# Optimization experiments

Measured on AMD Instinct MI355X. Metric: run time of the kernel, lower is better.

The kernel has to match this reference:

```python
import jax, jax.numpy as jnp
import numpy as np

EPS = 1e-5

def layer_norm(x, g, b):
    mu = jnp.mean(x, axis=-1, keepdims=True)
    var = jnp.mean(jnp.square(x - mu), axis=-1, keepdims=True)
    return (x - mu) * jax.lax.rsqrt(var + EPS) * g + b

def setup_inputs() -> dict:
    key = jax.random.key(0)
    B, N, IN_D, S, D = 64, 4096, 256, 8, 256
    ks = jax.random.split(key, 20)
    scale = lambda fan_in: 1.0 / np.sqrt(fan_in)
    u = lambda k, shape, s: jax.random.uniform(k, shape, jnp.float32, -s, s)
    return {
        "inputs": jax.random.normal(ks[0], (B, N, IN_D), jnp.float32),
        "noise": jax.random.normal(ks[1], (B, S, D), jnp.float32),
        "slots_mu": jax.random.normal(ks[2], (1, S, D), jnp.float32),
        "slots_sigma": jnp.ones((1, S, D), jnp.float32) * 0.1,
        "Wq": u(ks[3], (D, D), scale(D)), "bq": u(ks[4], (D,), scale(D)),
        "Wk": u(ks[5], (D, IN_D), scale(IN_D)), "bk": u(ks[6], (D,), scale(IN_D)),
        "Wv": u(ks[7], (D, IN_D), scale(IN_D)), "bv": u(ks[8], (D,), scale(IN_D)),
        "W_ih": u(ks[9], (3 * D, D), scale(D)), "b_ih": u(ks[10], (3 * D,), scale(D)),
        "W_hh": u(ks[11], (3 * D, D), scale(D)), "b_hh": u(ks[12], (3 * D,), scale(D)),
        "W1": u(ks[13], (D, D), scale(D)), "b1": u(ks[14], (D,), scale(D)),
        "W2": u(ks[15], (D, D), scale(D)), "b2": u(ks[16], (D,), scale(D)),
        "ln_slots_g": jnp.ones((D,), jnp.float32), "ln_slots_b": jnp.zeros((D,), jnp.float32),
        "ln_mlp_g": jnp.ones((D,), jnp.float32), "ln_mlp_b": jnp.zeros((D,), jnp.float32),
    }

def gru_cell(x, h, W_ih, b_ih, W_hh, b_hh):
    # PyTorch GRUCell: gates ordered (reset, update, new)
    gi = x @ W_ih.T + b_ih  # [B*S, 3D]
    gh = h @ W_hh.T + b_hh
    i_r, i_z, i_n = jnp.split(gi, 3, axis=-1)
    h_r, h_z, h_n = jnp.split(gh, 3, axis=-1)
    r = jax.nn.sigmoid(i_r + h_r)
    z = jax.nn.sigmoid(i_z + h_z)
    n = jnp.tanh(i_n + r * h_n)
    return (1.0 - z) * n + z * h

def reference(inputs, noise, slots_mu, slots_sigma, Wq, bq, Wk, bk, Wv, bv,
              W_ih, b_ih, W_hh, b_hh, W1, b1, W2, b2,
              ln_slots_g, ln_slots_b, ln_mlp_g, ln_mlp_b):
    B, N, _ = inputs.shape
    _, S, D = noise.shape
    num_iterations = 3
    slots = slots_mu + slots_sigma * noise  # [B, S, D]
    # k, v are loop-invariant; hoist the big GEMMs out of the iteration loop
    k = jnp.einsum('bnd,ed->bne', inputs, Wk) + bk  # [B, N, D]
    v = jnp.einsum('bnd,ed->bne', inputs, Wv) + bv  # [B, N, D]
    inv_sqrt_d = 1.0 / np.sqrt(D)
    for _ in range(num_iterations):
        slots_prev = slots
        q = layer_norm(slots, ln_slots_g, ln_slots_b) @ Wq.T + bq  # [B, S, D]
        attn_logits = jnp.einsum('bsd,bnd->bsn', q, k) * inv_sqrt_d
        attn = jax.nn.softmax(attn_logits, axis=-1)  # softmax over inputs (dim=-1)
        updates = jnp.einsum('bsn,bnd->bsd', attn, v)  # [B, S, D]
        h_new = gru_cell(updates.reshape(-1, D), slots_prev.reshape(-1, D),
                         W_ih, b_ih, W_hh, b_hh).reshape(B, S, D)
        slots = slots_prev + h_new  # residual around GRU (as in source)
        hidden = jax.nn.relu(layer_norm(slots, ln_mlp_g, ln_mlp_b) @ W1.T + b1)
        slots = slots + (hidden @ W2.T + b2)
    return slots
```

## Files before the change

kernel.cpp:

```cpp
#include <hip/hip_runtime.h>


constexpr int Bn = 64;
constexpr int Nn = 4096;
constexpr int Dd = 256;
constexpr int Ss = 8;
constexpr int CH = 16;
constexpr float EPSF = 1e-5f;

#define DEV __device__ __forceinline__

using short8 = __attribute__((ext_vector_type(8))) short;
using f32x4 = __attribute__((ext_vector_type(4))) float;
union U8 { short8 s; uint4 u; };

DEV unsigned bfpack2(float lo, float hi) {
  unsigned ul = __float_as_uint(lo), uh = __float_as_uint(hi);
  ul = (ul + 0x7FFFu + ((ul >> 16) & 1u)) >> 16;
  uh = (uh + 0x7FFFu + ((uh >> 16) & 1u)) & 0xFFFF0000u;
  return ul | uh;
}
DEV unsigned short bf16r(float x) {
  unsigned u = __float_as_uint(x);
  u = (u + 0x7FFFu + ((u >> 16) & 1u)) >> 16;
  return (unsigned short)u;
}
DEV float rsum32(float v) {
  v += __shfl_xor(v, 1); v += __shfl_xor(v, 2); v += __shfl_xor(v, 4);
  v += __shfl_xor(v, 8); v += __shfl_xor(v, 16);
  return v;
}
DEV float sigm(float x) { return 1.f / (1.f + __expf(-x)); }

template <int NK>
DEV void load_af(short8* a, const unsigned short* base, int lda, int m16, int quad) {
  const unsigned short* p = base + m16 * lda + quad * 8;
#pragma unroll
  for (int kk = 0; kk < NK; ++kk) a[kk] = *(const short8*)(p + kk * 32);
}
template <int NK>
DEV f32x4 gemm_tile(const short8* a, const unsigned short* wr, float binit) {
  f32x4 acc = {binit, binit, binit, binit};
#pragma unroll
  for (int kk = 0; kk < NK; ++kk) {
    short8 b = *(const short8*)(wr + kk * 32);
    acc = __builtin_amdgcn_mfma_f32_16x16x32_bf16(a[kk], b, acc, 0, 0, 0);
  }
  return acc;
}

DEV void ln_row8(const float* x, const float* g, const float* b, int d0,
                 unsigned short* dst) {
  float s = x[0] + x[1] + x[2] + x[3] + x[4] + x[5] + x[6] + x[7];
  float mu = rsum32(s) * (1.f / 256.f);
  float q = 0.f;
#pragma unroll
  for (int j = 0; j < 8; ++j) { float d = x[j] - mu; q += d * d; }
  float rs = rsqrtf(rsum32(q) * (1.f / 256.f) + EPSF);
  float o[8];
#pragma unroll
  for (int j = 0; j < 8; ++j) o[j] = (x[j] - mu) * rs * g[d0 + j] + b[d0 + j];
  uint4 w;
  w.x = bfpack2(o[0], o[1]); w.y = bfpack2(o[2], o[3]);
  w.z = bfpack2(o[4], o[5]); w.w = bfpack2(o[6], o[7]);
  *(uint4*)dst = w;
}

__global__ __launch_bounds__(256) void k_init(const float* __restrict__ noise,
                                              const float* __restrict__ mu,
                                              const float* __restrict__ sg,
                                              float* __restrict__ slots) {
  int i = blockIdx.x * 256 + threadIdx.x;
  float4 nz = ((const float4*)noise)[i];
  int m = i & 511;
  float4 m4 = ((const float4*)mu)[m];
  float4 s4 = ((const float4*)sg)[m];
  float4 o;
  o.x = m4.x + s4.x * nz.x; o.y = m4.y + s4.y * nz.y;
  o.z = m4.z + s4.z * nz.z; o.w = m4.w + s4.w * nz.w;
  ((float4*)slots)[i] = o;
}

__global__ __launch_bounds__(256) void k_wqk(const float* __restrict__ Wq,
                                             const float* __restrict__ Wk,
                                             const float* __restrict__ bq,
                                             float* __restrict__ WqkT,
                                             float* __restrict__ bqk) {
  int tid = threadIdx.x, c = blockIdx.x;
  if (c < 256) {
    float acc = 0.f;
    for (int e = 0; e < 256; ++e) acc += Wq[e * 256 + tid] * Wk[e * 256 + c];
    WqkT[c * 256 + tid] = acc;
  } else {
    float acc = 0.f;
    for (int e = 0; e < 256; ++e) acc += bq[e] * Wk[e * 256 + tid];
    bqk[tid] = acc;
  }
}

__global__ __launch_bounds__(256) void k_conv(
    const float* __restrict__ Wv, const float* __restrict__ Wih,
    const float* __restrict__ Whh, const float* __restrict__ W1,
    const float* __restrict__ W2, const float* __restrict__ WqkT,
    const float* __restrict__ bih, const float* __restrict__ bhh,
    unsigned* Wv_b, unsigned* Wzr_b, unsigned* Win_b, unsigned* Whn_b,
    unsigned* W1_b, unsigned* W2_b, unsigned* Wqk_b, float* bzr) {
  if (blockIdx.x >= 1280) {
    int i = (blockIdx.x - 1280) * 256 + threadIdx.x;
    if (i < 512) bzr[i] = bih[i] + bhh[i];
    return;
  }
  int p = blockIdx.x * 256 + threadIdx.x;
  const float* src; unsigned* dst;
  if (p < 32768) { src = Wv + 2 * p; dst = Wv_b + p; }
  else if (p < 163840) {
    int q = p - 32768, row = q >> 8, col = (q & 255) * 2;
    src = (col < 256) ? (Wih + row * 256 + col) : (Whh + row * 256 + col - 256);
    dst = Wzr_b + q;
  }
  else if (p < 196608) { int q = p - 163840; src = Wih + 512 * 256 + 2 * q; dst = Win_b + q; }
  else if (p < 229376) { int q = p - 196608; src = Whh + 512 * 256 + 2 * q; dst = Whn_b + q; }
  else if (p < 262144) { int q = p - 229376; src = W1 + 2 * q; dst = W1_b + q; }
  else if (p < 294912) { int q = p - 262144; src = W2 + 2 * q; dst = W2_b + q; }
  else { int q = p - 294912; src = WqkT + 2 * q; dst = Wqk_b + q; }
  dst[0] = bfpack2(src[0], src[1]);
}

__global__ __launch_bounds__(512) void k_qk0(const float* __restrict__ slots,
                                             const float* __restrict__ gsl,
                                             const float* __restrict__ bsl,
                                             const unsigned short* __restrict__ Wqk_b,
                                             const float* __restrict__ bqk,
                                             float* __restrict__ qk) {
  __shared__ __align__(16) unsigned short lnb[16 * 264];
  const int tid = threadIdx.x, bb = blockIdx.x;
  const int lane = tid & 63, wave = tid >> 6;
  const int m16 = lane & 15, quad = lane >> 4;
  const int row = tid >> 5, l32 = tid & 31, d0 = l32 * 8;
  {
    const float* sp = slots + (size_t)(bb * 16 + row) * 256 + d0;
    float4 v0 = *(const float4*)sp, v1 = *(const float4*)(sp + 4);
    float x[8] = {v0.x, v0.y, v0.z, v0.w, v1.x, v1.y, v1.z, v1.w};
    ln_row8(x, gsl, bsl, d0, lnb + row * 264 + d0);
  }
  __syncthreads();
  short8 a8[8];
  load_af<8>(a8, lnb, 264, m16, quad);
#pragma unroll
  for (int i = 0; i < 2; ++i) {
    int t = wave + 8 * i;
    f32x4 acc = gemm_tile<8>(a8, Wqk_b + (size_t)(t * 16 + m16) * 256 + quad * 8,
                             bqk[t * 16 + m16]);
#pragma unroll
    for (int r = 0; r < 4; ++r)
      qk[(size_t)(bb * 16 + quad * 4 + r) * 256 + t * 16 + m16] = acc[r] * 0.0625f;
  }
}

template <bool FIRST>
DEV void ld_chunk(const float* __restrict__ xin, unsigned* __restrict__ xbf,
                  size_t nbase, int tid, uint4* pr) {
#pragma unroll
  for (int i = 0; i < 4; ++i) {
    int flat = i * 256 + tid, n = flat >> 5, od = flat & 31;
    if (FIRST) {
      const float4* src = (const float4*)(xin + (nbase + n) * 256 + od * 8);
      float4 v0 = src[0], v1 = src[1];
      uint4 o;
      o.x = bfpack2(v0.x, v0.y); o.y = bfpack2(v0.z, v0.w);
      o.z = bfpack2(v1.x, v1.y); o.w = bfpack2(v1.z, v1.w);
      ((uint4*)xbf)[(nbase + n) * 32 + od] = o;
      pr[i] = o;
    } else {
      pr[i] = ((const uint4*)xbf)[(nbase + n) * 32 + od];
    }
  }
}

template <bool FIRST>
__global__ __launch_bounds__(256) void k_attn(const float* __restrict__ xin,
                                              unsigned* __restrict__ xbf,
                                              const float* __restrict__ qk,
                                              float* __restrict__ pl,
                                              float* __restrict__ pu) {
  __shared__ __align__(16) unsigned xt[2][128 * 33];
  __shared__ __align__(16) unsigned pp[16 * 17];
  __shared__ __align__(16) float lred[2][16];
  const int tid = threadIdx.x;
  const int lane = tid & 63, wave = tid >> 6;
  const int m16 = lane & 15, quad = lane >> 4;
  const int c = blockIdx.x, b = blockIdx.y;
  const int pb = (b * CH + c) * 8;

  short8 aq[8];
  {
    const float* qrow = qk + (size_t)(b * 8 + (m16 & 7)) * 256 + quad * 8;
#pragma unroll
    for (int kk = 0; kk < 8; ++kk) {
      U8 f;
      float4 q0 = *(const float4*)(qrow + kk * 32);
      float4 q1 = *(const float4*)(qrow + kk * 32 + 4);
      f.u.x = bfpack2(q0.x, q0.y); f.u.y = bfpack2(q0.z, q0.w);
      f.u.z = bfpack2(q1.x, q1.y); f.u.w = bfpack2(q1.z, q1.w);
      if (m16 >= 8) { f.u.x = 0u; f.u.y = 0u; f.u.z = 0u; f.u.w = 0u; }
      aq[kk] = f.s;
    }
  }
  float lacc[4] = {0.f, 0.f, 0.f, 0.f};
  f32x4 acc[4];
#pragma unroll
  for (int t = 0; t < 4; ++t) acc[t] = (f32x4){0.f, 0.f, 0.f, 0.f};
  const int d0w = wave * 64;

  uint4 pr[4];
  ld_chunk<FIRST>(xin, xbf, (size_t)b * Nn + (size_t)c * 256, tid, pr);

  for (int ch = 0; ch < 8; ++ch) {
    unsigned* xtb = xt[ch & 1];
#pragma unroll
    for (int i = 0; i < 4; ++i) {
      int flat = i * 256 + tid, n = flat >> 5, od = flat & 31, rb = od * 4;
      xtb[(rb + 0) * 33 + n] = pr[i].x;
      xtb[(rb + 1) * 33 + n] = pr[i].y;
      xtb[(rb + 2) * 33 + n] = pr[i].z;
      xtb[(rb + 3) * 33 + n] = pr[i].w;
    }
    __syncthreads();
    if (ch < 7)
      ld_chunk<FIRST>(xin, xbf, (size_t)b * Nn + (size_t)c * 256 + (ch + 1) * 32, tid, pr);
    if (wave < 2) {
      f32x4 pacc = (f32x4){0.f, 0.f, 0.f, 0.f};
#pragma unroll
      for (int kk = 0; kk < 8; ++kk) {
        int base = (kk * 16 + quad * 4) * 33 + wave * 16 + m16;
        U8 bf;
        bf.u.x = xtb[base]; bf.u.y = xtb[base + 33];
        bf.u.z = xtb[base + 66]; bf.u.w = xtb[base + 99];
        pacc = __builtin_amdgcn_mfma_f32_16x16x32_bf16(aq[kk], bf.s, pacc, 0, 0, 0);
      }
      const int xrow = wave * 16 + m16;
      unsigned short* pps = (unsigned short*)pp;
#pragma unroll
      for (int r = 0; r < 4; ++r) {
        float p = __expf(pacc[r]);
        lacc[r] += p;
        pps[((xrow >> 1) * 17 + quad * 4 + r) * 2 + (xrow & 1)] = bf16r(p);
      }
    }
    __syncthreads();
    U8 bp;
    bp.u.x = pp[(quad * 4 + 0) * 17 + m16];
    bp.u.y = pp[(quad * 4 + 1) * 17 + m16];
    bp.u.z = pp[(quad * 4 + 2) * 17 + m16];
    bp.u.w = pp[(quad * 4 + 3) * 17 + m16];
#pragma unroll
    for (int t = 0; t < 4; ++t) {
      int d = d0w + t * 16 + m16;
      int h = d >> 1, sel = d & 1;
      const unsigned* xr = xtb + h * 33 + quad * 8;
      unsigned u0 = xr[0], u1 = xr[1], u2 = xr[2], u3 = xr[3];
      unsigned u4 = xr[4], u5 = xr[5], u6 = xr[6], u7 = xr[7];
      U8 af;
      if (sel) {
        af.u.x = (u0 >> 16) | (u1 & 0xFFFF0000u);
        af.u.y = (u2 >> 16) | (u3 & 0xFFFF0000u);
        af.u.z = (u4 >> 16) | (u5 & 0xFFFF0000u);
        af.u.w = (u6 >> 16) | (u7 & 0xFFFF0000u);
      } else {
        af.u.x = (u0 & 0xFFFFu) | (u1 << 16);
        af.u.y = (u2 & 0xFFFFu) | (u3 << 16);
        af.u.z = (u4 & 0xFFFFu) | (u5 << 16);
        af.u.w = (u6 & 0xFFFFu) | (u7 << 16);
      }
      acc[t] = __builtin_amdgcn_mfma_f32_16x16x32_bf16(af.s, bp.s, acc[t], 0, 0, 0);
    }
    __syncthreads();
  }
  if (m16 < 8) {
#pragma unroll
    for (int t = 0; t < 4; ++t)
#pragma unroll
      for (int r = 0; r < 4; ++r)
        pu[(size_t)(pb + m16) * 256 + d0w + t * 16 + quad * 4 + r] = acc[t][r];
  }
  if (wave < 2) {
#pragma unroll
    for (int r = 0; r < 4; ++r) {
      float v = lacc[r];
      v += __shfl_xor(v, 1); v += __shfl_xor(v, 2);
      v += __shfl_xor(v, 4); v += __shfl_xor(v, 8);
      if (m16 == 0) lred[wave][quad * 4 + r] = v;
    }
  }
  __syncthreads();
  if (tid < 8) pl[pb + tid] = lred[0][tid] + lred[1][tid];
}

__global__ __launch_bounds__(512) void k_upd(
    const float* __restrict__ pl, const float* __restrict__ pu,
    const unsigned short* __restrict__ Wv_b, const float* __restrict__ bv,
    const unsigned short* __restrict__ Wzr_b, const float* __restrict__ bzr,
    const unsigned short* __restrict__ Win_b, const float* __restrict__ bin,
    const unsigned short* __restrict__ Whn_b, const float* __restrict__ bhn,
    const unsigned short* __restrict__ W1_b, const float* __restrict__ b1,
    const unsigned short* __restrict__ W2_b, const float* __restrict__ b2,
    const float* __restrict__ gml, const float* __restrict__ bml,
    const float* __restrict__ gsl, const float* __restrict__ bsl,
    const unsigned short* __restrict__ Wqk_b, const float* __restrict__ bqk,
    float* __restrict__ slots, float* __restrict__ qk, float* __restrict__ dout) {
  __shared__ __align__(16) unsigned short cat[16 * 520];
  __shared__ __align__(16) float sp[16 * 260];
  __shared__ __align__(16) float s1[16 * 260];
  __shared__ __align__(16) unsigned short lnb[16 * 264];
  const int tid = threadIdx.x, bb = blockIdx.x;
  const int lane = tid & 63, wave = tid >> 6;
  const int m16 = lane & 15, quad = lane >> 4;
  const int row = tid >> 5, l32 = tid & 31, d0 = l32 * 8;
  const int bat = 2 * bb + (row >> 3), sl = row & 7;
  {
    float L = 0.f;
#pragma unroll
    for (int cc = 0; cc < 16; ++cc) L += pl[(bat * 16 + cc) * 8 + sl];
    float li = 1.f / L;
    float a[8] = {0.f, 0.f, 0.f, 0.f, 0.f, 0.f, 0.f, 0.f};
    for (int cc = 0; cc < 16; ++cc) {
      const float* pp_ = pu + ((size_t)(bat * 16 + cc) * 8 + sl) * 256 + d0;
      float4 v0 = *(const float4*)pp_, v1 = *(const float4*)(pp_ + 4);
      a[0] += v0.x; a[1] += v0.y; a[2] += v0.z; a[3] += v0.w;
      a[4] += v1.x; a[5] += v1.y; a[6] += v1.z; a[7] += v1.w;
    }
    uint4 o;
    o.x = bfpack2(a[0] * li, a[1] * li); o.y = bfpack2(a[2] * li, a[3] * li);
    o.z = bfpack2(a[4] * li, a[5] * li); o.w = bfpack2(a[6] * li, a[7] * li);
    *(uint4*)(cat + row * 520 + d0) = o;
    const float* sp_ = slots + (size_t)(bb * 16 + row) * 256 + d0;
    float4 h0 = *(const float4*)sp_, h1 = *(const float4*)(sp_ + 4);
    *(float4*)(sp + row * 260 + d0) = h0;
    *(float4*)(sp + row * 260 + d0 + 4) = h1;
    uint4 hb;
    hb.x = bfpack2(h0.x, h0.y); hb.y = bfpack2(h0.z, h0.w);
    hb.z = bfpack2(h1.x, h1.y); hb.w = bfpack2(h1.z, h1.w);
    *(uint4*)(cat + row * 520 + 256 + d0) = hb;
  }
  __syncthreads();
  short8 afr[16];
  load_af<8>(afr, cat, 520, m16, quad);
  f32x4 accv[2];
#pragma unroll
  for (int i = 0; i < 2; ++i) {
    int t = wave + 8 * i;
    accv[i] = gemm_tile<8>(afr, Wv_b + (size_t)(t * 16 + m16) * 256 + quad * 8,
                           bv[t * 16 + m16]);
  }
  __syncthreads();
#pragma unroll
  for (int i = 0; i < 2; ++i) {
    int t = wave + 8 * i;
#pragma unroll
    for (int r = 0; r < 4; ++r)
      cat[(quad * 4 + r) * 520 + t * 16 + m16] = bf16r(accv[i][r]);
  }
  __syncthreads();
  load_af<16>(afr, cat, 520, m16, quad);
  f32x4 rr[2], zz[2];
#pragma unroll
  for (int i = 0; i < 2; ++i) {
    int t = wave + 8 * i;
    f32x4 ar = gemm_tile<16>(afr, Wzr_b + (size_t)(t * 16 + m16) * 512 + quad * 8,
                             bzr[t * 16 + m16]);
    f32x4 az = gemm_tile<16>(afr, Wzr_b + (size_t)((t + 16) * 16 + m16) * 512 + quad * 8,
                             bzr[(t + 16) * 16 + m16]);
#pragma unroll
    for (int r = 0; r < 4; ++r) { rr[i][r] = sigm(ar[r]); zz[i][r] = sigm(az[r]); }
  }
#pragma unroll
  for (int i = 0; i < 2; ++i) {
    int t = wave + 8 * i, col = t * 16 + m16;
    f32x4 ain = gemm_tile<8>(afr, Win_b + (size_t)(t * 16 + m16) * 256 + quad * 8,
                             bin[col]);
    f32x4 ahn = gemm_tile<8>(afr + 8, Whn_b + (size_t)(t * 16 + m16) * 256 + quad * 8,
                             bhn[col]);
#pragma unroll
    for (int r = 0; r < 4; ++r) {
      int rw = quad * 4 + r;
      float nin = ain[r] + rr[i][r] * ahn[r];
      float nn = 1.f - 2.f / (__expf(2.f * nin) + 1.f);
      float hpc = sp[rw * 260 + col];
      s1[rw * 260 + col] = hpc + (1.f - zz[i][r]) * nn + zz[i][r] * hpc;
    }
  }
  __syncthreads();
  {
    const float* s1r = s1 + row * 260 + d0;
    float4 v0 = *(const float4*)s1r, v1 = *(const float4*)(s1r + 4);
    float x[8] = {v0.x, v0.y, v0.z, v0.w, v1.x, v1.y, v1.z, v1.w};
    ln_row8(x, gml, bml, d0, lnb + row * 264 + d0);
  }
  __syncthreads();
  load_af<8>(afr, lnb, 264, m16, quad);
#pragma unroll
  for (int i = 0; i < 2; ++i) {
    int t = wave + 8 * i;
    f32x4 acc = gemm_tile<8>(afr, W1_b + (size_t)(t * 16 + m16) * 256 + quad * 8,
                             b1[t * 16 + m16]);
#pragma unroll
    for (int r = 0; r < 4; ++r)
      cat[(quad * 4 + r) * 520 + t * 16 + m16] = bf16r(fmaxf(acc[r], 0.f));
  }
  __syncthreads();
  load_af<8>(afr, cat, 520, m16, quad);
#pragma unroll
  for (int i = 0; i < 2; ++i) {
    int t = wave + 8 * i;
    f32x4 acc = gemm_tile<8>(afr, W2_b + (size_t)(t * 16 + m16) * 256 + quad * 8,
                             b2[t * 16 + m16]);
#pragma unroll
    for (int r = 0; r < 4; ++r) {
      int rw = quad * 4 + r, col = t * 16 + m16;
      float v = acc[r] + s1[rw * 260 + col];
      size_t gi = (size_t)(bb * 16 + rw) * 256 + col;
      slots[gi] = v;
      if (dout) dout[gi] = v;
      sp[rw * 260 + col] = v;
    }
  }
  __syncthreads();
  {
    const float* spr = sp + row * 260 + d0;
    float4 v0 = *(const float4*)spr, v1 = *(const float4*)(spr + 4);
    float x[8] = {v0.x, v0.y, v0.z, v0.w, v1.x, v1.y, v1.z, v1.w};
    ln_row8(x, gsl, bsl, d0, lnb + row * 264 + d0);
  }
  __syncthreads();
  load_af<8>(afr, lnb, 264, m16, quad);
#pragma unroll
  for (int i = 0; i < 2; ++i) {
    int t = wave + 8 * i;
    f32x4 acc = gemm_tile<8>(afr, Wqk_b + (size_t)(t * 16 + m16) * 256 + quad * 8,
                             bqk[t * 16 + m16]);
#pragma unroll
    for (int r = 0; r < 4; ++r)
      qk[(size_t)(bb * 16 + quad * 4 + r) * 256 + t * 16 + m16] = acc[r] * 0.0625f;
  }
}

extern "C" void kernel_launch(void* const* d_in, const int* in_sizes, int n_in,
                              void* d_out, int out_size, void* d_ws, size_t ws_size,
                              hipStream_t stream) {
  const float* inputs = (const float*)d_in[0];
  const float* noise = (const float*)d_in[1];
  const float* s_mu = (const float*)d_in[2];
  const float* s_sg = (const float*)d_in[3];
  const float* Wq = (const float*)d_in[4];
  const float* bq = (const float*)d_in[5];
  const float* Wk = (const float*)d_in[6];
  const float* Wv = (const float*)d_in[8];
  const float* bv = (const float*)d_in[9];
  const float* Wih = (const float*)d_in[10];
  const float* bih = (const float*)d_in[11];
  const float* Whh = (const float*)d_in[12];
  const float* bhh = (const float*)d_in[13];
  const float* W1 = (const float*)d_in[14];
  const float* b1 = (const float*)d_in[15];
  const float* W2 = (const float*)d_in[16];
  const float* b2 = (const float*)d_in[17];
  const float* gsl = (const float*)d_in[18];
  const float* bsl = (const float*)d_in[19];
  const float* gml = (const float*)d_in[20];
  const float* bml = (const float*)d_in[21];
  float* out = (float*)d_out;

  char* wsb = (char*)d_ws;
  unsigned* xbf = (unsigned*)wsb;
  float* fp = (float*)(wsb + (size_t)Bn * Nn * Dd * 2);
  float* slots = fp; fp += Bn * Ss * Dd;
  float* qk = fp;    fp += Bn * Ss * Dd;
  float* WqkT = fp;  fp += Dd * Dd;
  float* bqk = fp;   fp += Dd;
  float* pl = fp;    fp += Bn * CH * Ss;
  float* pu = fp;    fp += Bn * CH * Ss * Dd;
  float* bzr = fp;   fp += 512;
  unsigned short* wb = (unsigned short*)fp;
  unsigned short* Wv_b = wb;  wb += 65536;
  unsigned short* Wzr_b = wb; wb += 262144;
  unsigned short* Win_b = wb; wb += 65536;
  unsigned short* Whn_b = wb; wb += 65536;
  unsigned short* W1_b = wb;  wb += 65536;
  unsigned short* W2_b = wb;  wb += 65536;
  unsigned short* Wqk_b = wb; wb += 65536;
  (void)in_sizes; (void)n_in; (void)out_size; (void)ws_size;

  k_init<<<dim3(128), dim3(256), 0, stream>>>(noise, s_mu, s_sg, slots);
  k_wqk<<<dim3(257), dim3(256), 0, stream>>>(Wq, Wk, bq, WqkT, bqk);
  k_conv<<<dim3(1282), dim3(256), 0, stream>>>(
      Wv, Wih, Whh, W1, W2, WqkT, bih, bhh, (unsigned*)Wv_b, (unsigned*)Wzr_b,
      (unsigned*)Win_b, (unsigned*)Whn_b, (unsigned*)W1_b, (unsigned*)W2_b,
      (unsigned*)Wqk_b, bzr);
  k_qk0<<<dim3(32), dim3(512), 0, stream>>>(slots, gsl, bsl, Wqk_b, bqk, qk);
  for (int it = 0; it < 3; ++it) {
    if (it == 0)
      k_attn<true><<<dim3(CH, Bn), dim3(256), 0, stream>>>(inputs, xbf, qk, pl, pu);
    else
      k_attn<false><<<dim3(CH, Bn), dim3(256), 0, stream>>>(nullptr, xbf, qk, pl, pu);
    k_upd<<<dim3(32), dim3(512), 0, stream>>>(
        pl, pu, Wv_b, bv, Wzr_b, bzr, Win_b, bih + 512, Whn_b, bhh + 512, W1_b, b1,
        W2_b, b2, gml, bml, gsl, bsl, Wqk_b, bqk, slots, qk, (it == 2) ? out : nullptr);
  }
}
```

Measured before the change: 684.7 us.

## Warp-specialize attention kernel and fuse setup kernels

The attention kernel now splits its waves by role. Two waves compute the logits and exponentials for chunk ch into a double-buffered probability tile, while the other two waves run the P·V MFMAs for chunk ch-1, which removes one barrier per chunk. The byte-select logic uses v_perm. Slot initialisation is fused into k_qk0, and k_wqk writes the bf16 Wqk directly, which drops the k_init launch and the fp32 WqkT round trip. The risks are that half the waves now carry all the PV work with 8 accumulators each, and the pipeline adds an extra iteration.

```diff
diff --git a/kernel.cpp b/kernel.cpp
--- a/kernel.cpp
+++ b/kernel.cpp
@@ -66,31 +66,16 @@
   *(uint4*)dst = w;
 }
 
-__global__ __launch_bounds__(256) void k_init(const float* __restrict__ noise,
-                                              const float* __restrict__ mu,
-                                              const float* __restrict__ sg,
-                                              float* __restrict__ slots) {
-  int i = blockIdx.x * 256 + threadIdx.x;
-  float4 nz = ((const float4*)noise)[i];
-  int m = i & 511;
-  float4 m4 = ((const float4*)mu)[m];
-  float4 s4 = ((const float4*)sg)[m];
-  float4 o;
-  o.x = m4.x + s4.x * nz.x; o.y = m4.y + s4.y * nz.y;
-  o.z = m4.z + s4.z * nz.z; o.w = m4.w + s4.w * nz.w;
-  ((float4*)slots)[i] = o;
-}
-
 __global__ __launch_bounds__(256) void k_wqk(const float* __restrict__ Wq,
                                              const float* __restrict__ Wk,
                                              const float* __restrict__ bq,
-                                             float* __restrict__ WqkT,
+                                             unsigned short* __restrict__ Wqk_b,
                                              float* __restrict__ bqk) {
   int tid = threadIdx.x, c = blockIdx.x;
   if (c < 256) {
     float acc = 0.f;
     for (int e = 0; e < 256; ++e) acc += Wq[e * 256 + tid] * Wk[e * 256 + c];
-    WqkT[c * 256 + tid] = acc;
+    Wqk_b[c * 256 + tid] = bf16r(acc);
   } else {
     float acc = 0.f;
     for (int e = 0; e < 256; ++e) acc += bq[e] * Wk[e * 256 + tid];
@@ -101,12 +86,12 @@
 __global__ __launch_bounds__(256) void k_conv(
     const float* __restrict__ Wv, const float* __restrict__ Wih,
     const float* __restrict__ Whh, const float* __restrict__ W1,
-    const float* __restrict__ W2, const float* __restrict__ WqkT,
+    const float* __restrict__ W2,
     const float* __restrict__ bih, const float* __restrict__ bhh,
     unsigned* Wv_b, unsigned* Wzr_b, unsigned* Win_b, unsigned* Whn_b,
-    unsigned* W1_b, unsigned* W2_b, unsigned* Wqk_b, float* bzr) {
-  if (blockIdx.x >= 1280) {
-    int i = (blockIdx.x - 1280) * 256 + threadIdx.x;
+    unsigned* W1_b, unsigned* W2_b, float* bzr) {
+  if (blockIdx.x >= 1152) {
+    int i = (blockIdx.x - 1152) * 256 + threadIdx.x;
     if (i < 512) bzr[i] = bih[i] + bhh[i];
     return;
   }
@@ -121,16 +106,18 @@
   else if (p < 196608) { int q = p - 163840; src = Wih + 512 * 256 + 2 * q; dst = Win_b + q; }
   else if (p < 229376) { int q = p - 196608; src = Whh + 512 * 256 + 2 * q; dst = Whn_b + q; }
   else if (p < 262144) { int q = p - 229376; src = W1 + 2 * q; dst = W1_b + q; }
-  else if (p < 294912) { int q = p - 262144; src = W2 + 2 * q; dst = W2_b + q; }
-  else { int q = p - 294912; src = WqkT + 2 * q; dst = Wqk_b + q; }
+  else { int q = p - 262144; src = W2 + 2 * q; dst = W2_b + q; }
   dst[0] = bfpack2(src[0], src[1]);
 }
 
-__global__ __launch_bounds__(512) void k_qk0(const float* __restrict__ slots,
+__global__ __launch_bounds__(512) void k_qk0(const float* __restrict__ noise,
+                                             const float* __restrict__ s_mu,
+                                             const float* __restrict__ s_sg,
                                              const float* __restrict__ gsl,
                                              const float* __restrict__ bsl,
                                              const unsigned short* __restrict__ Wqk_b,
                                              const float* __restrict__ bqk,
+                                             float* __restrict__ slots,
                                              float* __restrict__ qk) {
   __shared__ __align__(16) unsigned short lnb[16 * 264];
   const int tid = threadIdx.x, bb = blockIdx.x;
@@ -138,9 +125,21 @@
   const int m16 = lane & 15, quad = lane >> 4;
   const int row = tid >> 5, l32 = tid & 31, d0 = l32 * 8;
   {
-    const float* sp = slots + (size_t)(bb * 16 + row) * 256 + d0;
-    float4 v0 = *(const float4*)sp, v1 = *(const float4*)(sp + 4);
-    float x[8] = {v0.x, v0.y, v0.z, v0.w, v1.x, v1.y, v1.z, v1.w};
+    const int grow = bb * 16 + row;
+    const int sidx = (grow & 7) * 256 + d0;
+    const float* np = noise + (size_t)grow * 256 + d0;
+    float4 n0 = *(const float4*)np, n1 = *(const float4*)(np + 4);
+    float4 m0 = *(const float4*)(s_mu + sidx), m1 = *(const float4*)(s_mu + sidx + 4);
+    float4 g0 = *(const float4*)(s_sg + sidx), g1 = *(const float4*)(s_sg + sidx + 4);
+    float x[8] = {m0.x + g0.x * n0.x, m0.y + g0.y * n0.y,
+                  m0.z + g0.z * n0.z, m0.w + g0.w * n0.w,
+                  m1.x + g1.x * n1.x, m1.y + g1.y * n1.y,
+                  m1.z + g1.z * n1.z, m1.w + g1.w * n1.w};
+    float* sp_ = slots + (size_t)grow * 256 + d0;
+    float4 o0, o1;
+    o0.x = x[0]; o0.y = x[1]; o0.z = x[2]; o0.w = x[3];
+    o1.x = x[4]; o1.y = x[5]; o1.z = x[6]; o1.w = x[7];
+    *(float4*)sp_ = o0; *(float4*)(sp_ + 4) = o1;
     ln_row8(x, gsl, bsl, d0, lnb + row * 264 + d0);
   }
   __syncthreads();
@@ -184,16 +183,18 @@
                                               float* __restrict__ pl,
                                               float* __restrict__ pu) {
   __shared__ __align__(16) unsigned xt[2][128 * 33];
-  __shared__ __align__(16) unsigned pp[16 * 17];
+  __shared__ __align__(16) unsigned pp[2][16 * 17];
   __shared__ __align__(16) float lred[2][16];
   const int tid = threadIdx.x;
   const int lane = tid & 63, wave = tid >> 6;
   const int m16 = lane & 15, quad = lane >> 4;
   const int c = blockIdx.x, b = blockIdx.y;
   const int pb = (b * CH + c) * 8;
+  const bool isA = (wave < 2);
+  const unsigned psel = (m16 & 1) ? 0x07060302u : 0x05040100u;
 
   short8 aq[8];
-  {
+  if (isA) {
     const float* qrow = qk + (size_t)(b * 8 + (m16 & 7)) * 256 + quad * 8;
 #pragma unroll
     for (int kk = 0; kk < 8; ++kk) {
@@ -207,83 +208,83 @@
     }
   }
   float lacc[4] = {0.f, 0.f, 0.f, 0.f};
-  f32x4 acc[4];
-#pragma unroll
-  for (int t = 0; t < 4; ++t) acc[t] = (f32x4){0.f, 0.f, 0.f, 0.f};
-  const int d0w = wave * 64;
+  f32x4 acc[8];
+#pragma unroll
+  for (int t = 0; t < 8; ++t) acc[t] = (f32x4){0.f, 0.f, 0.f, 0.f};
 
   uint4 pr[4];
-  ld_chunk<FIRST>(xin, xbf, (size_t)b * Nn + (size_t)c * 256, tid, pr);
-
-  for (int ch = 0; ch < 8; ++ch) {
-    unsigned* xtb = xt[ch & 1];
-#pragma unroll
-    for (int i = 0; i < 4; ++i) {
-      int flat = i * 256 + tid, n = flat >> 5, od = flat & 31, rb = od * 4;
-      xtb[(rb + 0) * 33 + n] = pr[i].x;
-      xtb[(rb + 1) * 33 + n] = pr[i].y;
-      xtb[(rb + 2) * 33 + n] = pr[i].z;
-      xtb[(rb + 3) * 33 + n] = pr[i].w;
+  const size_t nb0 = (size_t)b * Nn + (size_t)c * 256;
+  ld_chunk<FIRST>(xin, xbf, nb0, tid, pr);
+
+  for (int ch = 0; ch <= 8; ++ch) {
+    if (ch < 8) {
+      unsigned* xtb = xt[ch & 1];
+#pragma unroll
+      for (int i = 0; i < 4; ++i) {
+        int flat = i * 256 + tid, n = flat >> 5, od = flat & 31, rb = od * 4;
+        xtb[(rb + 0) * 33 + n] = pr[i].x;
+        xtb[(rb + 1) * 33 + n] = pr[i].y;
+        xtb[(rb + 2) * 33 + n] = pr[i].z;
+        xtb[(rb + 3) * 33 + n] = pr[i].w;
+      }
     }
     __syncthreads();
-    if (ch < 7)
-      ld_chunk<FIRST>(xin, xbf, (size_t)b * Nn + (size_t)c * 256 + (ch + 1) * 32, tid, pr);
-    if (wave < 2) {
-      f32x4 pacc = (f32x4){0.f, 0.f, 0.f, 0.f};
-#pragma unroll
-      for (int kk = 0; kk < 8; ++kk) {
-        int base = (kk * 16 + quad * 4) * 33 + wave * 16 + m16;
-        U8 bf;
-        bf.u.x = xtb[base]; bf.u.y = xtb[base + 33];
-        bf.u.z = xtb[base + 66]; bf.u.w = xtb[base + 99];
-        pacc = __builtin_amdgcn_mfma_f32_16x16x32_bf16(aq[kk], bf.s, pacc, 0, 0, 0);
+    if (ch + 1 < 8)
+      ld_chunk<FIRST>(xin, xbf, nb0 + (size_t)(ch + 1) * 32, tid, pr);
+    if (isA) {
+      if (ch < 8) {
+        const unsigned* xtb = xt[ch & 1];
+        f32x4 pacc = (f32x4){0.f, 0.f, 0.f, 0.f};
+#pragma unroll
+        for (int kk = 0; kk < 8; ++kk) {
+          int base = (kk * 16 + quad * 4) * 33 + wave * 16 + m16;
+          U8 bf;
+          bf.u.x = xtb[base]; bf.u.y = xtb[base + 33];
+          bf.u.z = xtb[base + 66]; bf.u.w = xtb[base + 99];
+          pacc = __builtin_amdgcn_mfma_f32_16x16x32_bf16(aq[kk], bf.s, pacc, 0, 0, 0);
+        }
+        const int xrow = wave * 16 + m16;
+        unsigned short* pps = (unsigned short*)pp[ch & 1];
+#pragma unroll
+        for (int r = 0; r < 4; ++r) {
+          float p = __expf(pacc[r]);
+          lacc[r] += p;
+          pps[((xrow >> 1) * 17 + quad * 4 + r) * 2 + (xrow & 1)] = bf16r(p);
+        }
       }
-      const int xrow = wave * 16 + m16;
-      unsigned short* pps = (unsigned short*)pp;
-#pragma unroll
-      for (int r = 0; r < 4; ++r) {
-        float p = __expf(pacc[r]);
-        lacc[r] += p;
-        pps[((xrow >> 1) * 17 + quad * 4 + r) * 2 + (xrow & 1)] = bf16r(p);
+    } else if (ch >= 1) {
+      const unsigned* xtb = xt[(ch - 1) & 1];
+      const unsigned* ppb = pp[(ch - 1) & 1];
+      U8 bp;
+      bp.u.x = ppb[(quad * 4 + 0) * 17 + m16];
+      bp.u.y = ppb[(quad * 4 + 1) * 17 + m16];
+      bp.u.z = ppb[(quad * 4 + 2) * 17 + m16];
+      bp.u.w = ppb[(quad * 4 + 3) * 17 + m16];
+#pragma unroll
+      for (int t = 0; t < 8; ++t) {
+        int d = (wave - 2) * 128 + t * 16 + m16;
+        const unsigned* xr = xtb + (d >> 1) * 33 + quad * 8;
+        unsigned u0 = xr[0], u1 = xr[1], u2 = xr[2], u3 = xr[3];
+        unsigned u4 = xr[4], u5 = xr[5], u6 = xr[6], u7 = xr[7];
+        U8 af;
+        af.u.x = __builtin_amdgcn_perm(u1, u0, psel);
+        af.u.y = __builtin_amdgcn_perm(u3, u2, psel);
+        af.u.z = __builtin_amdgcn_perm(u5, u4, psel);
+        af.u.w = __builtin_amdgcn_perm(u7, u6, psel);
+        acc[t] = __builtin_amdgcn_mfma_f32_16x16x32_bf16(af.s, bp.s, acc[t], 0, 0, 0);
       }
     }
     __syncthreads();
-    U8 bp;
-    bp.u.x = pp[(quad * 4 + 0) * 17 + m16];
-    bp.u.y = pp[(quad * 4 + 1) * 17 + m16];
-    bp.u.z = pp[(quad * 4 + 2) * 17 + m16];
-    bp.u.w = pp[(quad * 4 + 3) * 17 + m16];
-#pragma unroll
-    for (int t = 0; t < 4; ++t) {
-      int d = d0w + t * 16 + m16;
-      int h = d >> 1, sel = d & 1;
-      const unsigned* xr = xtb + h * 33 + quad * 8;
-      unsigned u0 = xr[0], u1 = xr[1], u2 = xr[2], u3 = xr[3];
-      unsigned u4 = xr[4], u5 = xr[5], u6 = xr[6], u7 = xr[7];
-      U8 af;
-      if (sel) {
-        af.u.x = (u0 >> 16) | (u1 & 0xFFFF0000u);
-        af.u.y = (u2 >> 16) | (u3 & 0xFFFF0000u);
-        af.u.z = (u4 >> 16) | (u5 & 0xFFFF0000u);
-        af.u.w = (u6 >> 16) | (u7 & 0xFFFF0000u);
-      } else {
-        af.u.x = (u0 & 0xFFFFu) | (u1 << 16);
-        af.u.y = (u2 & 0xFFFFu) | (u3 << 16);
-        af.u.z = (u4 & 0xFFFFu) | (u5 << 16);
-        af.u.w = (u6 & 0xFFFFu) | (u7 << 16);
-      }
-      acc[t] = __builtin_amdgcn_mfma_f32_16x16x32_bf16(af.s, bp.s, acc[t], 0, 0, 0);
-    }
-    __syncthreads();
-  }
-  if (m16 < 8) {
-#pragma unroll
-    for (int t = 0; t < 4; ++t)
+  }
+  if (!isA && m16 < 8) {
+    const int d0w = (wave - 2) * 128;
+#pragma unroll
+    for (int t = 0; t < 8; ++t)
 #pragma unroll
       for (int r = 0; r < 4; ++r)
         pu[(size_t)(pb + m16) * 256 + d0w + t * 16 + quad * 4 + r] = acc[t][r];
   }
-  if (wave < 2) {
+  if (isA) {
 #pragma unroll
     for (int r = 0; r < 4; ++r) {
       float v = lacc[r];
@@ -475,7 +476,6 @@
   float* fp = (float*)(wsb + (size_t)Bn * Nn * Dd * 2);
   float* slots = fp; fp += Bn * Ss * Dd;
   float* qk = fp;    fp += Bn * Ss * Dd;
-  float* WqkT = fp;  fp += Dd * Dd;
   float* bqk = fp;   fp += Dd;
   float* pl = fp;    fp += Bn * CH * Ss;
   float* pu = fp;    fp += Bn * CH * Ss * Dd;
@@ -490,13 +490,12 @@
   unsigned short* Wqk_b = wb; wb += 65536;
   (void)in_sizes; (void)n_in; (void)out_size; (void)ws_size;
 
-  k_init<<<dim3(128), dim3(256), 0, stream>>>(noise, s_mu, s_sg, slots);
-  k_wqk<<<dim3(257), dim3(256), 0, stream>>>(Wq, Wk, bq, WqkT, bqk);
-  k_conv<<<dim3(1282), dim3(256), 0, stream>>>(
-      Wv, Wih, Whh, W1, W2, WqkT, bih, bhh, (unsigned*)Wv_b, (unsigned*)Wzr_b,
-      (unsigned*)Win_b, (unsigned*)Whn_b, (unsigned*)W1_b, (unsigned*)W2_b,
-      (unsigned*)Wqk_b, bzr);
-  k_qk0<<<dim3(32), dim3(512), 0, stream>>>(slots, gsl, bsl, Wqk_b, bqk, qk);
+  k_wqk<<<dim3(257), dim3(256), 0, stream>>>(Wq, Wk, bq, Wqk_b, bqk);
+  k_conv<<<dim3(1154), dim3(256), 0, stream>>>(
+      Wv, Wih, Whh, W1, W2, bih, bhh, (unsigned*)Wv_b, (unsigned*)Wzr_b,
+      (unsigned*)Win_b, (unsigned*)Whn_b, (unsigned*)W1_b, (unsigned*)W2_b, bzr);
+  k_qk0<<<dim3(32), dim3(512), 0, stream>>>(noise, s_mu, s_sg, gsl, bsl, Wqk_b, bqk,
+                                            slots, qk);
   for (int it = 0; it < 3; ++it) {
     if (it == 0)
       k_attn<true><<<dim3(CH, Bn), dim3(256), 0, stream>>>(inputs, xbf, qk, pl, pu);
```

Result: no change. 679.6 us (-0.7%).
